# Optimization experiments

Measured on AMD Instinct MI355X. Metric: run time of the kernel, lower is better.

Reference implementation:

```python
import jax, jax.numpy as jnp
import numpy as np

HEIGHT, WIDTH, NUM_FRAMES, DIM = 64, 64, 16, 1280
GRIDS = [(8, 32, 32), (16, 16, 16), (4, 48, 48), (1, 64, 64)]  # ragged (t,h,w) per sample


def _sincos_1d(embed_dim, t_size):
    # matches get_1d_sincos_pos_embed_from_grid
    omega = np.arange(embed_dim // 2, dtype=np.float32) / (embed_dim / 2.0)
    omega = 1.0 / (10000.0 ** omega)
    pos = np.arange(t_size, dtype=np.float32)
    out = np.einsum('m,d->md', pos, omega)
    return np.concatenate([np.sin(out), np.cos(out)], axis=1).astype(np.float32)  # [t, dim]


def setup_inputs() -> dict:
    key = jax.random.key(0)
    k1, k2 = jax.random.split(key)
    total_tokens = sum(t * h * w for t, h, w in GRIDS)  # 25600
    x = jax.random.normal(k1, (total_tokens, DIM), dtype=jnp.float32)
    weight = jax.random.normal(k2, (HEIGHT, WIDTH, DIM), dtype=jnp.float32)  # learnable 2D pos emb
    time_weight = jnp.asarray(_sincos_1d(DIM, NUM_FRAMES))  # [num_frames, dim] sincos buffer
    grid_thws = np.asarray(GRIDS, dtype=np.int64)  # static per-sample (t,h,w)
    return {"x": x, "weight": weight, "time_weight": time_weight, "grid_thws": grid_thws}


def reference(x, weight, time_weight, grid_thws):
    H, W, D = weight.shape
    grids = np.asarray(grid_thws).tolist()  # static metadata; loop is over ragged samples
    pos_embs = []
    for t, h, w in grids:
        if (h, w) == (H, W):
            pe2d = weight.reshape(-1, D)  # [h*w, D]
        else:
            # torch path: fp32 bicubic interpolation of [H,W,D] -> [h,w,D]
            pe2d = jax.image.resize(weight.astype(jnp.float32), (h, w, D),
                                    method='bicubic').astype(x.dtype).reshape(-1, D)
        if t == 1:
            pe3d = pe2d
        else:
            # broadcast-add temporal sincos embedding: [t,1,D] + [1,h*w,D]
            pe3d = (pe2d[None, :, :] + time_weight[:t, None, :]).reshape(-1, D)
        pos_embs.append(pe3d)
    return x + jnp.concatenate(pos_embs, axis=0)
```

## Files before the change

### kernel.cpp

```cpp
#include <hip/hip_runtime.h>


#define TMP32_OFF 0
#define TMP16_OFF 2621440
#define TMP48_OFF 3932160
#define PE32_OFF  7864320
#define PE16_OFF  9175040
#define PE48_OFF  9502720

__device__ __forceinline__ float keys_cubic(float x) {
    x = fabsf(x);
    if (x >= 2.0f) return 0.0f;
    if (x >= 1.0f) return ((-0.5f * x + 2.5f) * x - 4.0f) * x + 2.0f;
    return ((1.5f * x - 2.5f) * x) * x + 1.0f;
}

__device__ __forceinline__ void tap_params(int o, int out_size,
                                           int& i0, int& n, float& sf,
                                           float& inv_ks, float& inv_sum) {
    float inv_scale = 64.0f / (float)out_size;
    float ks = inv_scale;
    float radius = 2.0f * ks;
    sf = ((float)o + 0.5f) * inv_scale - 0.5f;
    int lo = (int)ceilf(sf - radius); if (lo < 0) lo = 0;
    int hi = (int)floorf(sf + radius); if (hi > 63) hi = 63;
    n = hi - lo + 1;
    i0 = lo;
    inv_ks = 1.0f / ks;
    float sum = 0.0f;
    for (int k = 0; k < n; ++k)
        sum += keys_cubic((sf - (float)(lo + k)) * inv_ks);
    inv_sum = 1.0f / sum;
}

__global__ __launch_bounds__(320) void resize_h_kernel(const float* __restrict__ weight,
                                                       float* __restrict__ ws) {
    int bid = blockIdx.x;
    int out_h, oy, x;
    float* dst;
    if (bid < 2048)      { out_h = 32; int b = bid;        oy = b >> 6; x = b & 63;
                           dst = ws + TMP32_OFF + (size_t)(oy * 64 + x) * 1280; }
    else if (bid < 3072) { out_h = 16; int b = bid - 2048; oy = b >> 6; x = b & 63;
                           dst = ws + TMP16_OFF + (size_t)(oy * 64 + x) * 1280; }
    else                 { out_h = 48; int b = bid - 3072; oy = b >> 6; x = b & 63;
                           dst = ws + TMP48_OFF + (size_t)(oy * 64 + x) * 1280; }

    int i0, n; float sf, inv_ks, inv_sum;
    tap_params(oy, out_h, i0, n, sf, inv_ks, inv_sum);

    int d = threadIdx.x << 2;
    const float* src = weight + (size_t)x * 1280 + d;
    float4 acc = make_float4(0.f, 0.f, 0.f, 0.f);
    for (int k = 0; k < n; ++k) {
        float c = keys_cubic((sf - (float)(i0 + k)) * inv_ks);
        float4 v = *(const float4*)(src + (size_t)(i0 + k) * (64 * 1280));
        acc.x += c * v.x; acc.y += c * v.y; acc.z += c * v.z; acc.w += c * v.w;
    }
    acc.x *= inv_sum; acc.y *= inv_sum; acc.z *= inv_sum; acc.w *= inv_sum;
    *(float4*)(dst + d) = acc;
}

__global__ __launch_bounds__(320) void resize_w_kernel(float* __restrict__ ws) {
    int bid = blockIdx.x;
    int out_w, oy, ox;
    const float* src_base; float* dst;
    if (bid < 1024)      { out_w = 32; int b = bid;        oy = b >> 5; ox = b & 31;
                           src_base = ws + TMP32_OFF;
                           dst = ws + PE32_OFF + (size_t)(oy * 32 + ox) * 1280; }
    else if (bid < 1280) { out_w = 16; int b = bid - 1024; oy = b >> 4; ox = b & 15;
                           src_base = ws + TMP16_OFF;
                           dst = ws + PE16_OFF + (size_t)(oy * 16 + ox) * 1280; }
    else                 { out_w = 48; int b = bid - 1280; oy = b / 48; ox = b - oy * 48;
                           src_base = ws + TMP48_OFF;
                           dst = ws + PE48_OFF + (size_t)(oy * 48 + ox) * 1280; }

    int j0, n; float sf, inv_ks, inv_sum;
    tap_params(ox, out_w, j0, n, sf, inv_ks, inv_sum);

    int d = threadIdx.x << 2;
    const float* src = src_base + (size_t)(oy * 64) * 1280 + d;
    float4 acc = make_float4(0.f, 0.f, 0.f, 0.f);
    for (int k = 0; k < n; ++k) {
        float c = keys_cubic((sf - (float)(j0 + k)) * inv_ks);
        float4 v = *(const float4*)(src + (size_t)(j0 + k) * 1280);
        acc.x += c * v.x; acc.y += c * v.y; acc.z += c * v.z; acc.w += c * v.w;
    }
    acc.x *= inv_sum; acc.y *= inv_sum; acc.z *= inv_sum; acc.w *= inv_sum;
    *(float4*)(dst + d) = acc;
}

__global__ __launch_bounds__(256) void add_pe_kernel(const float* __restrict__ x,
                                                     const float* __restrict__ weight,
                                                     const float* __restrict__ tw,
                                                     const float* __restrict__ ws,
                                                     float* __restrict__ out) {
    int v = blockIdx.x * 256 + threadIdx.x;
    int token = v / 320;
    int d = (v - token * 320) << 2;

    const float* pe;
    int frame;
    if (token < 8192) {
        frame = token >> 10;
        int px = token & 1023;
        pe = ws + PE32_OFF + (size_t)px * 1280;
    } else if (token < 12288) {
        int l = token - 8192;
        frame = l >> 8;
        int px = l & 255;
        pe = ws + PE16_OFF + (size_t)px * 1280;
    } else if (token < 21504) {
        int l = token - 12288;
        frame = l / 2304;
        int px = l - frame * 2304;
        pe = ws + PE48_OFF + (size_t)px * 1280;
    } else {
        int l = token - 21504;
        frame = -1;
        pe = weight + (size_t)l * 1280;
    }

    size_t off = (size_t)token * 1280 + d;
    float4 xv = *(const float4*)(x + off);
    float4 pv = *(const float4*)(pe + d);
    float4 o = make_float4(xv.x + pv.x, xv.y + pv.y, xv.z + pv.z, xv.w + pv.w);
    if (frame >= 0) {
        float4 tv = *(const float4*)(tw + (size_t)frame * 1280 + d);
        o.x += tv.x; o.y += tv.y; o.z += tv.z; o.w += tv.w;
    }
    *(float4*)(out + off) = o;
}

extern "C" void kernel_launch(void* const* d_in, const int* in_sizes, int n_in,
                              void* d_out, int out_size, void* d_ws, size_t ws_size,
                              hipStream_t stream) {
    const float* x      = (const float*)d_in[0];
    const float* weight = (const float*)d_in[1];
    const float* tw     = (const float*)d_in[2];
    float* ws  = (float*)d_ws;
    float* out = (float*)d_out;

    hipLaunchKernelGGL(resize_h_kernel, dim3(6144), dim3(320), 0, stream, weight, ws);
    hipLaunchKernelGGL(resize_w_kernel, dim3(3584), dim3(320), 0, stream, ws);
    hipLaunchKernelGGL(add_pe_kernel, dim3(32000), dim3(256), 0, stream, x, weight, tw, ws, out);
}
```

Before: 277.5 us.

## Fuse separable bicubic resize passes into one kernel using LDS intermediate

```diff
diff --git a/kernel.cpp b/kernel.cpp
--- a/kernel.cpp
+++ b/kernel.cpp
@@ -1,12 +1,9 @@
 #include <hip/hip_runtime.h>
 
 
-#define TMP32_OFF 0
-#define TMP16_OFF 2621440
-#define TMP48_OFF 3932160
-#define PE32_OFF  7864320
-#define PE16_OFF  9175040
-#define PE48_OFF  9502720
+#define PE32_OFF 0
+#define PE16_OFF 1310720
+#define PE48_OFF 1638400
 
 __device__ __forceinline__ float keys_cubic(float x) {
     x = fabsf(x);
@@ -33,60 +30,52 @@
     inv_sum = 1.0f / sum;
 }
 
-__global__ __launch_bounds__(320) void resize_h_kernel(const float* __restrict__ weight,
+#define TMP_STRIDE 68
+__global__ __launch_bounds__(256) void resize2d_kernel(const float* __restrict__ weight,
                                                        float* __restrict__ ws) {
-    int bid = blockIdx.x;
-    int out_h, oy, x;
-    float* dst;
-    if (bid < 2048)      { out_h = 32; int b = bid;        oy = b >> 6; x = b & 63;
-                           dst = ws + TMP32_OFF + (size_t)(oy * 64 + x) * 1280; }
-    else if (bid < 3072) { out_h = 16; int b = bid - 2048; oy = b >> 6; x = b & 63;
-                           dst = ws + TMP16_OFF + (size_t)(oy * 64 + x) * 1280; }
-    else                 { out_h = 48; int b = bid - 3072; oy = b >> 6; x = b & 63;
-                           dst = ws + TMP48_OFF + (size_t)(oy * 64 + x) * 1280; }
+    int td  = blockIdx.x % 20;
+    int row = blockIdx.x / 20;
+    int out_h, out_w, oy; float* pe_base;
+    if (row < 32)      { out_h = 32; out_w = 32; oy = row;      pe_base = ws + PE32_OFF; }
+    else if (row < 48) { out_h = 16; out_w = 16; oy = row - 32; pe_base = ws + PE16_OFF; }
+    else               { out_h = 48; out_w = 48; oy = row - 48; pe_base = ws + PE48_OFF; }
+    int d0 = td * 64;
 
-    int i0, n; float sf, inv_ks, inv_sum;
-    tap_params(oy, out_h, i0, n, sf, inv_ks, inv_sum);
+    __shared__ float tmp[64 * TMP_STRIDE];
 
-    int d = threadIdx.x << 2;
-    const float* src = weight + (size_t)x * 1280 + d;
-    float4 acc = make_float4(0.f, 0.f, 0.f, 0.f);
-    for (int k = 0; k < n; ++k) {
-        float c = keys_cubic((sf - (float)(i0 + k)) * inv_ks);
-        float4 v = *(const float4*)(src + (size_t)(i0 + k) * (64 * 1280));
-        acc.x += c * v.x; acc.y += c * v.y; acc.z += c * v.z; acc.w += c * v.w;
+    int i0, nh; float sfh, ikh, ish;
+    tap_params(oy, out_h, i0, nh, sfh, ikh, ish);
+
+    for (int item = threadIdx.x; item < 1024; item += 256) {
+        int x  = item >> 4;
+        int f4 = item & 15;
+        const float* src = weight + (size_t)x * 1280 + d0 + (f4 << 2);
+        float4 acc = make_float4(0.f, 0.f, 0.f, 0.f);
+        for (int k = 0; k < nh; ++k) {
+            float c = keys_cubic((sfh - (float)(i0 + k)) * ikh);
+            float4 v = *(const float4*)(src + (size_t)(i0 + k) * (64 * 1280));
+            acc.x += c * v.x; acc.y += c * v.y; acc.z += c * v.z; acc.w += c * v.w;
+        }
+        acc.x *= ish; acc.y *= ish; acc.z *= ish; acc.w *= ish;
+        *(float4*)&tmp[x * TMP_STRIDE + (f4 << 2)] = acc;
     }
-    acc.x *= inv_sum; acc.y *= inv_sum; acc.z *= inv_sum; acc.w *= inv_sum;
-    *(float4*)(dst + d) = acc;
-}
+    __syncthreads();
 
-__global__ __launch_bounds__(320) void resize_w_kernel(float* __restrict__ ws) {
-    int bid = blockIdx.x;
-    int out_w, oy, ox;
-    const float* src_base; float* dst;
-    if (bid < 1024)      { out_w = 32; int b = bid;        oy = b >> 5; ox = b & 31;
-                           src_base = ws + TMP32_OFF;
-                           dst = ws + PE32_OFF + (size_t)(oy * 32 + ox) * 1280; }
-    else if (bid < 1280) { out_w = 16; int b = bid - 1024; oy = b >> 4; ox = b & 15;
-                           src_base = ws + TMP16_OFF;
-                           dst = ws + PE16_OFF + (size_t)(oy * 16 + ox) * 1280; }
-    else                 { out_w = 48; int b = bid - 1280; oy = b / 48; ox = b - oy * 48;
-                           src_base = ws + TMP48_OFF;
-                           dst = ws + PE48_OFF + (size_t)(oy * 48 + ox) * 1280; }
-
-    int j0, n; float sf, inv_ks, inv_sum;
-    tap_params(ox, out_w, j0, n, sf, inv_ks, inv_sum);
-
-    int d = threadIdx.x << 2;
-    const float* src = src_base + (size_t)(oy * 64) * 1280 + d;
-    float4 acc = make_float4(0.f, 0.f, 0.f, 0.f);
-    for (int k = 0; k < n; ++k) {
-        float c = keys_cubic((sf - (float)(j0 + k)) * inv_ks);
-        float4 v = *(const float4*)(src + (size_t)(j0 + k) * 1280);
-        acc.x += c * v.x; acc.y += c * v.y; acc.z += c * v.z; acc.w += c * v.w;
+    int nitems = out_w << 4;
+    for (int item = threadIdx.x; item < nitems; item += 256) {
+        int ox = item >> 4;
+        int f4 = item & 15;
+        int j0, nw; float sfw, ikw, isw;
+        tap_params(ox, out_w, j0, nw, sfw, ikw, isw);
+        float4 acc = make_float4(0.f, 0.f, 0.f, 0.f);
+        for (int k = 0; k < nw; ++k) {
+            float c = keys_cubic((sfw - (float)(j0 + k)) * ikw);
+            float4 v = *(const float4*)&tmp[(j0 + k) * TMP_STRIDE + (f4 << 2)];
+            acc.x += c * v.x; acc.y += c * v.y; acc.z += c * v.z; acc.w += c * v.w;
+        }
+        acc.x *= isw; acc.y *= isw; acc.z *= isw; acc.w *= isw;
+        *(float4*)(pe_base + (size_t)(oy * out_w + ox) * 1280 + d0 + (f4 << 2)) = acc;
     }
-    acc.x *= inv_sum; acc.y *= inv_sum; acc.z *= inv_sum; acc.w *= inv_sum;
-    *(float4*)(dst + d) = acc;
 }
 
 __global__ __launch_bounds__(256) void add_pe_kernel(const float* __restrict__ x,
@@ -140,7 +129,6 @@
     float* ws  = (float*)d_ws;
     float* out = (float*)d_out;
 
-    hipLaunchKernelGGL(resize_h_kernel, dim3(6144), dim3(320), 0, stream, weight, ws);
-    hipLaunchKernelGGL(resize_w_kernel, dim3(3584), dim3(320), 0, stream, ws);
+    hipLaunchKernelGGL(resize2d_kernel, dim3(1920), dim3(256), 0, stream, weight, ws);
     hipLaunchKernelGGL(add_pe_kernel, dim3(32000), dim3(256), 0, stream, x, weight, tw, ws, out);
 }
```

Result: faster. 266.5 us (-4.0%).
